# Optimization experiments

Measured on AMD Instinct MI355X. Metric: run time of the kernel, lower is better.

## Reference

```python
import jax, jax.numpy as jnp
import numpy as np

N = 20000   # nodes
E = 320000  # edges
F0 = 32     # num_features
H = 8       # GAT heads
G = 64      # graphs in batch


def setup_inputs() -> dict:
    key = jax.random.key(0)
    ks = jax.random.split(key, 16)
    def p(k, shape, s=0.05):
        return jax.random.normal(k, shape, jnp.float32) * s
    d = {}
    d['x'] = jax.random.normal(ks[0], (N, F0), jnp.float32)
    d['edge_index'] = jax.random.randint(ks[1], (2, E), 0, N, dtype=jnp.int32)
    d['edge_weights'] = jax.random.uniform(ks[2], (E,), jnp.float32)
    d['batch'] = jnp.sort(jax.random.randint(ks[3], (N,), 0, G, dtype=jnp.int32))
    # GATConv(32 -> 32, heads=8)
    d['W_gat'] = p(ks[4], (F0, H * F0)); d['att_src'] = p(ks[5], (H, F0))
    d['att_dst'] = p(ks[6], (H, F0));    d['b_gat'] = jnp.zeros((H * F0,), jnp.float32)
    # residual Linear(256 -> 1024) (widened so the residual add is shape-consistent)
    d['W_res'] = p(ks[7], (H * F0, 1024)); d['b_res'] = jnp.zeros((1024,), jnp.float32)
    # GCNConv(256 -> 512) + BN1
    d['W2'] = p(ks[8], (H * F0, 512)); d['b2'] = jnp.zeros((512,), jnp.float32)
    d['g1'] = jnp.ones((512,), jnp.float32); d['be1'] = jnp.zeros((512,), jnp.float32)
    d['m1'] = jnp.zeros((512,), jnp.float32); d['v1'] = jnp.ones((512,), jnp.float32)
    # GCNConv(512 -> 1024) + BN2
    d['W3'] = p(ks[9], (512, 1024)); d['b3'] = jnp.zeros((1024,), jnp.float32)
    d['g2'] = jnp.ones((1024,), jnp.float32); d['be2'] = jnp.zeros((1024,), jnp.float32)
    d['m2'] = jnp.zeros((1024,), jnp.float32); d['v2'] = jnp.ones((1024,), jnp.float32)
    # head
    d['Wf1'] = p(ks[10], (1024, 256)); d['bf1'] = jnp.zeros((256,), jnp.float32)
    d['Wf2'] = p(ks[11], (256, 2));    d['bf2'] = jnp.zeros((2,), jnp.float32)
    return d


def _add_self_loops(edge_index, edge_weight, n):
    loop = jnp.arange(n, dtype=edge_index.dtype)
    ei = jnp.concatenate([edge_index, jnp.stack([loop, loop])], axis=1)
    ew = jnp.concatenate([edge_weight, jnp.ones((n,), edge_weight.dtype)])
    return ei, ew


def _gat(x, edge_index, W, att_src, att_dst, b, n):
    # PyG GATConv, concat=True, eval (attention dropout off). Self-loops already added.
    src, dst = edge_index[0], edge_index[1]
    h = (x @ W).reshape(n, H, -1)                    # [N,H,C]
    a_s = jnp.einsum('nhc,hc->nh', h, att_src)        # [N,H]
    a_d = jnp.einsum('nhc,hc->nh', h, att_dst)
    e = jax.nn.leaky_relu(a_s[src] + a_d[dst], 0.2)   # [E,H]
    m = jax.ops.segment_max(e, dst, num_segments=n)   # softmax over incoming edges
    ex = jnp.exp(e - m[dst])
    s = jax.ops.segment_sum(ex, dst, num_segments=n)
    alpha = ex / s[dst]
    out = jax.ops.segment_sum(h[src] * alpha[:, :, None], dst, num_segments=n)
    return out.reshape(n, -1) + b                     # [N,H*C]


def _gcn(x, edge_index, w, W, b, n):
    # PyG GCNConv with symmetric normalization; self-loops (weight 1) already added.
    src, dst = edge_index[0], edge_index[1]
    deg = jax.ops.segment_sum(w, dst, num_segments=n)
    dinv = jnp.where(deg > 0, jax.lax.rsqrt(jnp.maximum(deg, 1e-12)), 0.0)
    norm = dinv[src] * w * dinv[dst]                  # [E]
    h = x @ W                                         # transform first (cheaper)
    return jax.ops.segment_sum(h[src] * norm[:, None], dst, num_segments=n) + b


def _bn(x, g, b, m, v):
    return g * (x - m) * jax.lax.rsqrt(v + 1e-5) + b


def reference(x, edge_index, edge_weights, batch, W_gat, att_src, att_dst, b_gat,
              W_res, b_res, W2, b2, g1, be1, m1, v1, W3, b3, g2, be2, m2, v2,
              Wf1, bf1, Wf2, bf2):
    n = x.shape[0]
    ei, ew = _add_self_loops(edge_index, edge_weights, n)
    h = jax.nn.relu(_gat(x, ei, W_gat, att_src, att_dst, b_gat, n))   # [N,256]
    res = h @ W_res + b_res                                           # [N,1024]
    h = _gcn(h, ei, ew, W2, b2, n)                                    # [N,512]
    h = jax.nn.relu(_bn(h, g1, be1, m1, v1))
    h = _gcn(h, ei, ew, W3, b3, n)                                    # [N,1024]
    h = jax.nn.relu(_bn(h, g2, be2, m2, v2))
    h = h + res
    pooled = jax.ops.segment_max(h, batch, num_segments=G)            # global max pool [G,1024]
    z = jax.nn.relu(pooled @ Wf1 + bf1)                               # dropout is eval no-op
    return z @ Wf2 + bf2                                              # [G,2]
```

## Files before the change

kernel.cpp:

```cpp
#include <hip/hip_runtime.h>
#include <hip/hip_bf16.h>

#define NN 20000
#define EE 320000
#define GG 64
#define EN (EE + NN)
#define MT 157

typedef float f32x4 __attribute__((ext_vector_type(4)));
typedef __bf16 bf16x4 __attribute__((ext_vector_type(4)));
typedef __bf16 bf16x8 __attribute__((ext_vector_type(8)));

__device__ __forceinline__ void gl_lds16(const void* g, void* l) {
    __builtin_amdgcn_global_load_lds((const __attribute__((address_space(1))) void*)g,
                                     (__attribute__((address_space(3))) void*)l, 16, 0, 0);
}

__global__ void sentinel_kernel(float* out, int n) {
    int i = blockIdx.x * 256 + threadIdx.x;
    if (i < n) out[i] = 12345.0f;
}

__global__ void init_kernel(int* deg_cnt, float* deg_w, int* fill, float* pooled) {
    int i = blockIdx.x * 256 + threadIdx.x;
    if (i < NN) { deg_cnt[i] = 1; deg_w[i] = 1.0f; fill[i] = 0; }
    if (i < GG * 1024) pooled[i] = -INFINITY;
}

__global__ __launch_bounds__(256) void convert_wt(const float* __restrict__ W, __bf16* __restrict__ Wt,
                                                  int K, int N) {
    __shared__ float tile[64][65];
    int kb = blockIdx.y * 64, nb = blockIdx.x * 64;
    int tx = threadIdx.x & 63, ty = threadIdx.x >> 6;
#pragma unroll
    for (int i = ty; i < 64; i += 4)
        tile[i][tx] = W[(size_t)(kb + i) * N + nb + tx];
    __syncthreads();
#pragma unroll
    for (int i = ty; i < 64; i += 4)
        Wt[(size_t)(nb + i) * K + kb + tx] = (__bf16)tile[tx][i];
}

__global__ __launch_bounds__(256) void gat_transform(
    const float* __restrict__ x, const float* __restrict__ W,
    const float* __restrict__ att_s, const float* __restrict__ att_d,
    __bf16* __restrict__ hlin, float* __restrict__ a_s, float* __restrict__ a_d)
{
    __shared__ float Ws[32 * 256];
    int tid = threadIdx.x;
#pragma unroll
    for (int k = 0; k < 32; k++) Ws[k * 256 + tid] = W[k * 256 + tid];
    float asc = att_s[tid], adc = att_d[tid];
    __syncthreads();
    for (int n = blockIdx.x; n < NN; n += gridDim.x) {
        const float* xp = x + (size_t)n * 32;
        float acc = 0.f;
#pragma unroll
        for (int k = 0; k < 32; k++) acc += xp[k] * Ws[k * 256 + tid];
        hlin[(size_t)n * 256 + tid] = (__bf16)acc;
        float s = acc * asc, d = acc * adc;
#pragma unroll
        for (int m = 1; m <= 16; m <<= 1) { s += __shfl_xor(s, m); d += __shfl_xor(d, m); }
        if ((tid & 31) == 0) { int h = tid >> 5; a_s[n * 8 + h] = s; a_d[n * 8 + h] = d; }
    }
}

__global__ void deg_kernel(const int* __restrict__ ei, const float* __restrict__ ew,
                           int* deg_cnt, float* deg_w) {
    int e = blockIdx.x * 256 + threadIdx.x;
    if (e >= EE) return;
    int dst = ei[EE + e];
    atomicAdd(&deg_cnt[dst], 1);
    atomicAdd(&deg_w[dst], ew[e]);
}

__global__ __launch_bounds__(256) void scan_kernel(const int* __restrict__ deg_cnt, int* __restrict__ rowptr) {
    __shared__ int partial[256];
    int tid = threadIdx.x;
    const int chunk = (NN + 255) / 256;
    int s0 = tid * chunk, s1 = min(s0 + chunk, NN);
    int sum = 0;
    for (int i = s0; i < s1; i++) sum += deg_cnt[i];
    partial[tid] = sum;
    __syncthreads();
    if (tid == 0) {
        int run = 0;
        for (int i = 0; i < 256; i++) { int t = partial[i]; partial[i] = run; run += t; }
        rowptr[NN] = run;
    }
    __syncthreads();
    int run = partial[tid];
    for (int i = s0; i < s1; i++) { rowptr[i] = run; run += deg_cnt[i]; }
}

__global__ void fill_kernel(const int* __restrict__ ei, const float* __restrict__ ew,
                            const float* __restrict__ deg_w, const int* __restrict__ rowptr,
                            int* fill, int* __restrict__ csr_src, float* __restrict__ csr_norm) {
    int e = blockIdx.x * 256 + threadIdx.x;
    if (e >= EN) return;
    int src, dst; float w;
    if (e < EE) { src = ei[e]; dst = ei[EE + e]; w = ew[e]; }
    else        { src = dst = e - EE; w = 1.0f; }
    int pos = atomicAdd(&fill[dst], 1);
    int slot = rowptr[dst] + pos;
    csr_src[slot] = src;
    csr_norm[slot] = rsqrtf(deg_w[src]) * w * rsqrtf(deg_w[dst]);
}

__global__ __launch_bounds__(256) void gat_agg(
    const int* __restrict__ rowptr, const int* __restrict__ csr_src,
    const float* __restrict__ a_s, const float* __restrict__ a_d,
    const __bf16* __restrict__ hlin, const float* __restrict__ b_gat,
    __bf16* __restrict__ h1)
{
    int widx = threadIdx.x >> 6, lane = threadIdx.x & 63;
    int node = blockIdx.x * 4 + widx;
    int base = rowptr[node], deg = rowptr[node + 1] - base;
    int hA = lane & 7;
    int eslot = lane >> 3;
    int hB = lane >> 3;
    float adA = a_d[node * 8 + hA];
    float acc0[4] = {0.f, 0.f, 0.f, 0.f};
    float acc1[4] = {0.f, 0.f, 0.f, 0.f};

    if (deg <= 64) {
        int sv = (lane < deg) ? csr_src[base + lane] : 0;
        float ev[8];
        float psum = 0.f;
#pragma unroll
        for (int j = 0; j < 8; j++) {
            int e = j * 8 + eslot;
            float v = 0.f;
            if (e < deg) {
                int src = __shfl(sv, e);
                float t = a_s[src * 8 + hA] + adA;
                t = (t > 0.f) ? t : 0.2f * t;
                v = __expf(t);
            }
            ev[j] = v;
            psum += v;
        }
#pragma unroll
        for (int m = 8; m <= 32; m <<= 1) psum += __shfl_xor(psum, m);
        float sinv = 1.f / __shfl(psum, hB);
#pragma unroll
        for (int j = 0; j < 8; j++) {
            if (j * 8 >= deg) break;
            int lim = min(8, deg - j * 8);
            int t = 0;
            for (; t + 1 < lim; t += 2) {
                int s0 = j * 8 + t, s1 = s0 + 1;
                int srcA = __shfl(sv, s0), srcB = __shfl(sv, s1);
                float aA = __shfl(ev[j], (t << 3) | hB) * sinv;
                float aB = __shfl(ev[j], ((t + 1) << 3) | hB) * sinv;
                bf16x4 fA = *(const bf16x4*)(hlin + (size_t)srcA * 256 + lane * 4);
                bf16x4 fB = *(const bf16x4*)(hlin + (size_t)srcB * 256 + lane * 4);
#pragma unroll
                for (int c = 0; c < 4; c++) { acc0[c] += aA * (float)fA[c]; acc1[c] += aB * (float)fB[c]; }
            }
            if (t < lim) {
                int s0 = j * 8 + t;
                int src = __shfl(sv, s0);
                float alpha = __shfl(ev[j], (t << 3) | hB) * sinv;
                bf16x4 f = *(const bf16x4*)(hlin + (size_t)src * 256 + lane * 4);
#pragma unroll
                for (int c = 0; c < 4; c++) acc0[c] += alpha * (float)f[c];
            }
        }
    } else {
        float sum = 0.f;
        for (int e = 0; e < deg; e++) {
            int src = csr_src[base + e];
            float t = a_s[src * 8 + hA] + adA;
            t = (t > 0.f) ? t : 0.2f * t;
            sum += __expf(t);
        }
        float sinv = 1.f / __shfl(sum, hB);
        float adB = a_d[node * 8 + hB];
        for (int e = 0; e < deg; e++) {
            int src = csr_src[base + e];
            float t = a_s[src * 8 + hB] + adB;
            t = (t > 0.f) ? t : 0.2f * t;
            float alpha = __expf(t) * sinv;
            bf16x4 f = *(const bf16x4*)(hlin + (size_t)src * 256 + lane * 4);
#pragma unroll
            for (int c = 0; c < 4; c++) acc0[c] += alpha * (float)f[c];
        }
    }
    float4 bg = *(const float4*)(b_gat + lane * 4);
    bf16x4 o;
    o[0] = (__bf16)fmaxf(acc0[0] + acc1[0] + bg.x, 0.f);
    o[1] = (__bf16)fmaxf(acc0[1] + acc1[1] + bg.y, 0.f);
    o[2] = (__bf16)fmaxf(acc0[2] + acc1[2] + bg.z, 0.f);
    o[3] = (__bf16)fmaxf(acc0[3] + acc1[3] + bg.w, 0.f);
    *(bf16x4*)(h1 + (size_t)node * 256 + lane * 4) = o;
}

template <int C, int SPLIT>
__global__ __launch_bounds__(256) void gcn_agg(
    const int* __restrict__ rowptr, const int* __restrict__ csr_src,
    const float* __restrict__ csr_norm, const __bf16* __restrict__ feat,
    __bf16* __restrict__ out)
{
    constexpr int V = C / (64 * SPLIT);
    int widx = threadIdx.x >> 6, lane = threadIdx.x & 63;
    int node = blockIdx.x * (4 / SPLIT) + widx / SPLIT;
    int half = widx % SPLIT;
    int coff = half * (C / SPLIT) + lane * V;
    int base = rowptr[node], deg = rowptr[node + 1] - base;
    float acc0[V], acc1[V], acc2[V], acc3[V];
#pragma unroll
    for (int j = 0; j < V; j++) { acc0[j] = 0.f; acc1[j] = 0.f; acc2[j] = 0.f; acc3[j] = 0.f; }
    const __bf16* fb = feat + coff;
    typedef __bf16 bf16v __attribute__((ext_vector_type(V)));
    for (int e0 = 0; e0 < deg; e0 += 64) {
        int cnt = min(64, deg - e0);
        int sv = 0; float wv = 0.f;
        if (lane < cnt) { sv = csr_src[base + e0 + lane]; wv = csr_norm[base + e0 + lane]; }
        int s = 0;
        for (; s + 3 < cnt; s += 4) {
            int sA = __shfl(sv, s),     sB = __shfl(sv, s + 1);
            int sC = __shfl(sv, s + 2), sD = __shfl(sv, s + 3);
            float wA = __shfl(wv, s),     wB = __shfl(wv, s + 1);
            float wC = __shfl(wv, s + 2), wD = __shfl(wv, s + 3);
            bf16v fA = *(const bf16v*)(fb + (size_t)sA * C);
            bf16v fB = *(const bf16v*)(fb + (size_t)sB * C);
            bf16v fC = *(const bf16v*)(fb + (size_t)sC * C);
            bf16v fD = *(const bf16v*)(fb + (size_t)sD * C);
#pragma unroll
            for (int j = 0; j < V; j++) {
                acc0[j] += wA * (float)fA[j]; acc1[j] += wB * (float)fB[j];
                acc2[j] += wC * (float)fC[j]; acc3[j] += wD * (float)fD[j];
            }
        }
        for (; s < cnt; s++) {
            int src = __shfl(sv, s);
            float w = __shfl(wv, s);
            bf16v f = *(const bf16v*)(fb + (size_t)src * C);
#pragma unroll
            for (int j = 0; j < V; j++) acc0[j] += w * (float)f[j];
        }
    }
    bf16v o;
#pragma unroll
    for (int j = 0; j < V; j++) o[j] = (__bf16)((acc0[j] + acc1[j]) + (acc2[j] + acc3[j]));
    *(bf16v*)(out + (size_t)node * C + coff) = o;
}


__device__ __forceinline__ void stage_async64(
    const __bf16* __restrict__ A, int K, const __bf16* __restrict__ Wt,
    int bm, int bn, int k0, int tid, __bf16* As, __bf16* Bs)
{
#pragma unroll
    for (int i = 0; i < 4; i++) {
        int j = i * 256 + tid;
        int r = j >> 3, c = j & 7;
        const __bf16* gp = A + (size_t)(bm + r) * K + k0 + ((c ^ (r & 7)) * 8);
        gl_lds16(gp, As + (size_t)(j & ~63) * 8);
    }
#pragma unroll
    for (int i = 0; i < 4; i++) {
        int j = i * 256 + tid;
        int r = j >> 3, c = j & 7;
        const __bf16* gp = Wt + (size_t)(bn + r) * K + k0 + ((c ^ (r & 7)) * 8);
        gl_lds16(gp, Bs + (size_t)(j & ~63) * 8);
    }
}

__device__ __forceinline__ void mfma_step64(
    const __bf16* As, const __bf16* Bs, int wr, int wc, int l16, int q, f32x4 (&acc)[4][4])
{
#pragma unroll
    for (int ks = 0; ks < 2; ks++) {
        bf16x8 af[4], bfv[4];
#pragma unroll
        for (int mt = 0; mt < 4; mt++) {
            int row = wr * 64 + mt * 16 + l16;
            af[mt] = *(const bf16x8*)(As + row * 64 + (((ks * 4 + q) ^ (row & 7)) * 8));
        }
#pragma unroll
        for (int nt = 0; nt < 4; nt++) {
            int row = wc * 64 + nt * 16 + l16;
            bfv[nt] = *(const bf16x8*)(Bs + row * 64 + (((ks * 4 + q) ^ (row & 7)) * 8));
        }
#pragma unroll
        for (int mt = 0; mt < 4; mt++)
#pragma unroll
            for (int nt = 0; nt < 4; nt++)
                acc[mt][nt] = __builtin_amdgcn_mfma_f32_16x16x32_bf16(af[mt], bfv[nt], acc[mt][nt], 0, 0, 0);
    }
}

__device__ __forceinline__ void gemm_loop(
    const __bf16* __restrict__ A, int K, const __bf16* __restrict__ Wt,
    int bm, int bn, int tid, int wr, int wc, int l16, int q,
    __bf16* As, __bf16* Bs, f32x4 (&acc)[4][4])
{
    for (int k0 = 0; k0 < K; k0 += 64) {
        stage_async64(A, K, Wt, bm, bn, k0, tid, As, Bs);
        __syncthreads();
        mfma_step64(As, Bs, wr, wc, l16, q, acc);
        __syncthreads();
    }
}

__global__ __launch_bounds__(256) void gemm_bn_relu(
    const __bf16* __restrict__ A, const __bf16* __restrict__ Wt,
    int M, int K, int Nc,
    const float* __restrict__ bias,
    const float* __restrict__ g, const float* __restrict__ be,
    const float* __restrict__ mu, const float* __restrict__ var,
    __bf16* __restrict__ C)
{
    __shared__ __bf16 As[128 * 64];
    __shared__ __bf16 Bs[128 * 64];
    int tid = threadIdx.x;
    int w = tid >> 6, wr = w >> 1, wc = w & 1;
    int l = tid & 63, q = l >> 4, l16 = l & 15;
    int i = blockIdx.x;
    int k = (i & 3) * MT + (i >> 2);
    int bm = (k >> 2) * 128, bn = (k & 3) * 128;
    f32x4 acc[4][4] = {};
    gemm_loop(A, K, Wt, bm, bn, tid, wr, wc, l16, q, As, Bs, acc);
#pragma unroll
    for (int nt = 0; nt < 4; nt++) {
        int gn = bn + wc * 64 + nt * 16 + l16;
        float s = g[gn] * rsqrtf(var[gn] + 1e-5f);
        float t = be[gn] - mu[gn] * s;
        float bv = bias[gn];
#pragma unroll
        for (int mt = 0; mt < 4; mt++)
#pragma unroll
            for (int r = 0; r < 4; r++) {
                int gm = bm + wr * 64 + mt * 16 + q * 4 + r;
                if (gm < M) C[(size_t)gm * Nc + gn] = (__bf16)fmaxf((acc[mt][nt][r] + bv) * s + t, 0.f);
            }
    }
}

__device__ __forceinline__ void atomicMaxFloat(float* addr, float value) {
    if (value >= 0.f) atomicMax((int*)addr, __float_as_int(value));
    else              atomicMin((unsigned int*)addr, __float_as_uint(value));
}

__global__ __launch_bounds__(256) void gemm_final(
    const __bf16* __restrict__ A1, const __bf16* __restrict__ W3t,
    const __bf16* __restrict__ A2, const __bf16* __restrict__ Wrt,
    const float* __restrict__ b3, const float* __restrict__ bres,
    const float* __restrict__ g, const float* __restrict__ be,
    const float* __restrict__ mu, const float* __restrict__ var,
    const int* __restrict__ batch, float* __restrict__ pooled)
{
    const int M = NN;
    __shared__ __bf16 As[128 * 64];
    __shared__ __bf16 Bs[128 * 64];
    __shared__ int bat[128];
    int tid = threadIdx.x;
    int w = tid >> 6, wr = w >> 1, wc = w & 1;
    int l = tid & 63, q = l >> 4, l16 = l & 15;
    int i = blockIdx.x;
    int k = (i & 7) * MT + (i >> 3);
    int bm = (k >> 3) * 128, bn = (k & 7) * 128;
    if (tid < 128) bat[tid] = (bm + tid < M) ? batch[bm + tid] : -1;
    f32x4 acc[4][4] = {};
    f32x4 accR[4][4] = {};
    gemm_loop(A1, 512, W3t, bm, bn, tid, wr, wc, l16, q, As, Bs, acc);
    gemm_loop(A2, 256, Wrt, bm, bn, tid, wr, wc, l16, q, As, Bs, accR);
#pragma unroll
    for (int nt = 0; nt < 4; nt++) {
        int gn = bn + wc * 64 + nt * 16 + l16;
        float s = g[gn] * rsqrtf(var[gn] + 1e-5f);
        float t = be[gn] - mu[gn] * s;
        float bv3 = b3[gn];
        float bvr = bres[gn];
        int cb = -1; float run = 0.f;
#pragma unroll
        for (int mt = 0; mt < 4; mt++)
#pragma unroll
            for (int r = 0; r < 4; r++) {
                int lr = wr * 64 + mt * 16 + q * 4 + r;
                int id = bat[lr];
                if (id < 0) continue;
                float v = fmaxf((acc[mt][nt][r] + bv3) * s + t, 0.f) + accR[mt][nt][r] + bvr;
                if (id == cb) run = fmaxf(run, v);
                else {
                    if (cb >= 0) atomicMaxFloat(&pooled[cb * 1024 + gn], run);
                    cb = id; run = v;
                }
            }
        if (cb >= 0) atomicMaxFloat(&pooled[cb * 1024 + gn], run);
    }
}

__global__ __launch_bounds__(256) void head_kernel(
    const float* __restrict__ pooled, const float* __restrict__ Wf1, const float* __restrict__ bf1,
    const float* __restrict__ Wf2, const float* __restrict__ bf2, float* __restrict__ out)
{
    int gph = blockIdx.x, tid = threadIdx.x;
    __shared__ float prow[1024];
    __shared__ float zred[256];
    for (int i = tid; i < 1024; i += 256) prow[i] = pooled[gph * 1024 + i];
    __syncthreads();
    float z = 0.f;
    for (int k = 0; k < 1024; k++) z += prow[k] * Wf1[k * 256 + tid];
    z = fmaxf(z + bf1[tid], 0.f);
    for (int c = 0; c < 2; c++) {
        zred[tid] = z * Wf2[tid * 2 + c];
        __syncthreads();
        for (int s = 128; s > 0; s >>= 1) { if (tid < s) zred[tid] += zred[tid + s]; __syncthreads(); }
        if (tid == 0) out[gph * 2 + c] = zred[0] + bf2[c];
        __syncthreads();
    }
}

extern "C" void kernel_launch(void* const* d_in, const int* in_sizes, int n_in,
                              void* d_out, int out_size, void* d_ws, size_t ws_size,
                              hipStream_t stream) {
    const float* x       = (const float*)d_in[0];
    const int*   ei      = (const int*)d_in[1];
    const float* ew      = (const float*)d_in[2];
    const int*   batch   = (const int*)d_in[3];
    const float* W_gat   = (const float*)d_in[4];
    const float* att_src = (const float*)d_in[5];
    const float* att_dst = (const float*)d_in[6];
    const float* b_gat   = (const float*)d_in[7];
    const float* W_res   = (const float*)d_in[8];
    const float* b_res   = (const float*)d_in[9];
    const float* W2      = (const float*)d_in[10];
    const float* b2v     = (const float*)d_in[11];
    const float* g1      = (const float*)d_in[12];
    const float* be1     = (const float*)d_in[13];
    const float* m1      = (const float*)d_in[14];
    const float* v1      = (const float*)d_in[15];
    const float* W3      = (const float*)d_in[16];
    const float* b3      = (const float*)d_in[17];
    const float* g2      = (const float*)d_in[18];
    const float* be2     = (const float*)d_in[19];
    const float* m2      = (const float*)d_in[20];
    const float* v2      = (const float*)d_in[21];
    const float* Wf1     = (const float*)d_in[22];
    const float* bf1     = (const float*)d_in[23];
    const float* Wf2     = (const float*)d_in[24];
    const float* bf2v    = (const float*)d_in[25];
    float* out           = (float*)d_out;

    char* ws = (char*)d_ws;
    size_t off = 0;
    auto alloc = [&](size_t bytes) { size_t o = off; off += (bytes + 255) & ~(size_t)255; return o; };
    size_t o_hlin   = alloc((size_t)NN * 256 * 2);
    size_t o_h1     = alloc((size_t)NN * 256 * 2);
    size_t o_h2     = alloc((size_t)NN * 512 * 2);
    size_t o_agg2   = alloc((size_t)NN * 512 * 2);
    size_t o_as     = alloc((size_t)NN * 8 * 4);
    size_t o_ad     = alloc((size_t)NN * 8 * 4);
    size_t o_degc   = alloc((size_t)NN * 4);
    size_t o_degw   = alloc((size_t)NN * 4);
    size_t o_rowptr = alloc((size_t)(NN + 1) * 4);
    size_t o_fill   = alloc((size_t)NN * 4);
    size_t o_csrs   = alloc((size_t)EN * 4);
    size_t o_csrn   = alloc((size_t)EN * 4);
    size_t o_pool   = alloc((size_t)GG * 1024 * 4);
    size_t o_w2t    = alloc((size_t)512 * 256 * 2);
    size_t o_w3t    = alloc((size_t)1024 * 512 * 2);
    size_t o_wrt    = alloc((size_t)1024 * 256 * 2);
    if (off > ws_size) {
        sentinel_kernel<<<(out_size + 255) / 256, 256, 0, stream>>>(out, out_size);
        return;
    }

    __bf16* hlin   = (__bf16*)(ws + o_hlin);
    __bf16* agg1   = hlin;
    __bf16* h1     = (__bf16*)(ws + o_h1);
    __bf16* h2     = (__bf16*)(ws + o_h2);
    __bf16* agg2   = (__bf16*)(ws + o_agg2);
    float*  a_s    = (float*)(ws + o_as);
    float*  a_d    = (float*)(ws + o_ad);
    int*    degc   = (int*)(ws + o_degc);
    float*  degw   = (float*)(ws + o_degw);
    int*    rowptr = (int*)(ws + o_rowptr);
    int*    fillb  = (int*)(ws + o_fill);
    int*    csrs   = (int*)(ws + o_csrs);
    float*  csrn   = (float*)(ws + o_csrn);
    float*  pooled = (float*)(ws + o_pool);
    __bf16* W2t    = (__bf16*)(ws + o_w2t);
    __bf16* W3t    = (__bf16*)(ws + o_w3t);
    __bf16* Wrt    = (__bf16*)(ws + o_wrt);

    init_kernel<<<256, 256, 0, stream>>>(degc, degw, fillb, pooled);
    convert_wt<<<dim3(512 / 64, 256 / 64), 256, 0, stream>>>(W2, W2t, 256, 512);
    convert_wt<<<dim3(1024 / 64, 512 / 64), 256, 0, stream>>>(W3, W3t, 512, 1024);
    convert_wt<<<dim3(1024 / 64, 256 / 64), 256, 0, stream>>>(W_res, Wrt, 256, 1024);

    gat_transform<<<512, 256, 0, stream>>>(x, W_gat, att_src, att_dst, hlin, a_s, a_d);
    deg_kernel<<<(EE + 255) / 256, 256, 0, stream>>>(ei, ew, degc, degw);
    scan_kernel<<<1, 256, 0, stream>>>(degc, rowptr);
    fill_kernel<<<(EN + 255) / 256, 256, 0, stream>>>(ei, ew, degw, rowptr, fillb, csrs, csrn);
    gat_agg<<<NN / 4, 256, 0, stream>>>(rowptr, csrs, a_s, a_d, hlin, b_gat, h1);

    gcn_agg<256, 1><<<NN / 4, 256, 0, stream>>>(rowptr, csrs, csrn, h1, agg1);
    gemm_bn_relu<<<4 * MT, 256, 0, stream>>>(agg1, W2t, NN, 256, 512, b2v,
        g1, be1, m1, v1, h2);
    gcn_agg<512, 2><<<NN / 2, 256, 0, stream>>>(rowptr, csrs, csrn, h2, agg2);
    gemm_final<<<8 * MT, 256, 0, stream>>>(agg2, W3t, h1, Wrt,
        b3, b_res, g2, be2, m2, v2, batch, pooled);

    head_kernel<<<GG, 256, 0, stream>>>(pooled, Wf1, bf1, Wf2, bf2v, out);
}
```

Before: 445.0 us.

## Fuse graph preprocessing into one cooperative kernel and merge weight conversions

Replaces the init, degree-count, scan and CSR-fill kernels with a single cooperative kernel that separates phases with grid-wide syncs, and parallelises the scan across 256 blocks instead of one. The three weight transpose/convert launches are merged into one launch that picks its matrix by block index. The aim is to cut kernel launch overhead and the serial single-block scan. In exchange it adds several grid barriers on a 256-block grid and limits the degree and fill loops to a fixed grid-stride launch.

Result: slower. 667.0 us (+49.9%).

```diff
diff --git a/kernel.cpp b/kernel.cpp
--- a/kernel.cpp
+++ b/kernel.cpp
@@ -1,11 +1,15 @@
 #include <hip/hip_runtime.h>
 #include <hip/hip_bf16.h>
+#include <hip/hip_cooperative_groups.h>
+
+namespace cg = cooperative_groups;
 
 #define NN 20000
 #define EE 320000
 #define GG 64
 #define EN (EE + NN)
 #define MT 157
+#define NPB 79
 
 typedef float f32x4 __attribute__((ext_vector_type(4)));
 typedef __bf16 bf16x4 __attribute__((ext_vector_type(4)));
@@ -21,16 +25,90 @@
     if (i < n) out[i] = 12345.0f;
 }
 
-__global__ void init_kernel(int* deg_cnt, float* deg_w, int* fill, float* pooled) {
-    int i = blockIdx.x * 256 + threadIdx.x;
-    if (i < NN) { deg_cnt[i] = 1; deg_w[i] = 1.0f; fill[i] = 0; }
-    if (i < GG * 1024) pooled[i] = -INFINITY;
-}
-
-__global__ __launch_bounds__(256) void convert_wt(const float* __restrict__ W, __bf16* __restrict__ Wt,
-                                                  int K, int N) {
+__global__ __launch_bounds__(256) void preproc_kernel(
+    int* __restrict__ deg_cnt, float* __restrict__ deg_w, int* __restrict__ fillc,
+    float* __restrict__ pooled,
+    const int* __restrict__ ei, const float* __restrict__ ew,
+    int* __restrict__ rowptr, int* __restrict__ bsum,
+    int* __restrict__ csr_src, float* __restrict__ csr_norm)
+{
+    cg::grid_group grid = cg::this_grid();
+    int tid = threadIdx.x, b = blockIdx.x;
+    int gtid = b * 256 + tid, gstride = 256 * 256;
+    __shared__ int red[256];
+    __shared__ int loc[NPB + 1];
+
+    for (int i = gtid; i < NN; i += gstride) { deg_cnt[i] = 1; deg_w[i] = 1.0f; fillc[i] = 0; }
+    for (int i = gtid; i < GG * 1024; i += gstride) pooled[i] = -INFINITY;
+    __threadfence();
+    grid.sync();
+
+    for (int e = gtid; e < EE; e += gstride) {
+        int dst = ei[EE + e];
+        atomicAdd(&deg_cnt[dst], 1);
+        atomicAdd(&deg_w[dst], ew[e]);
+    }
+    __threadfence();
+    grid.sync();
+
+    {
+        int s0 = b * NPB;
+        int v = 0;
+        if (tid < NPB && s0 + tid < NN) v = deg_cnt[s0 + tid];
+        red[tid] = v;
+        __syncthreads();
+        for (int s = 128; s > 0; s >>= 1) { if (tid < s) red[tid] += red[tid + s]; __syncthreads(); }
+        if (tid == 0) bsum[b] = red[0];
+    }
+    __threadfence();
+    grid.sync();
+
+    if (b == 0) {
+        if (tid == 0) {
+            int run = 0;
+            for (int i = 0; i < 256; i++) { int t = bsum[i]; bsum[i] = run; run += t; }
+            rowptr[NN] = run;
+        }
+    }
+    __threadfence();
+    grid.sync();
+
+    {
+        int s0 = b * NPB;
+        if (tid < NPB && s0 + tid < NN) loc[tid] = deg_cnt[s0 + tid];
+        __syncthreads();
+        if (tid == 0) {
+            int run = bsum[b];
+            for (int i = 0; i < NPB; i++) { int t = (s0 + i < NN) ? loc[i] : 0; loc[i] = run; run += t; }
+        }
+        __syncthreads();
+        if (tid < NPB && s0 + tid < NN) rowptr[s0 + tid] = loc[tid];
+    }
+    __threadfence();
+    grid.sync();
+
+    for (int e = gtid; e < EN; e += gstride) {
+        int src, dst; float w;
+        if (e < EE) { src = ei[e]; dst = ei[EE + e]; w = ew[e]; }
+        else        { src = dst = e - EE; w = 1.0f; }
+        int pos = atomicAdd(&fillc[dst], 1);
+        int slot = rowptr[dst] + pos;
+        csr_src[slot] = src;
+        csr_norm[slot] = rsqrtf(deg_w[src]) * w * rsqrtf(deg_w[dst]);
+    }
+}
+
+__global__ __launch_bounds__(256) void convert_all(
+    const float* __restrict__ W2, const float* __restrict__ W3, const float* __restrict__ Wres,
+    __bf16* __restrict__ W2t, __bf16* __restrict__ W3t, __bf16* __restrict__ Wrt)
+{
     __shared__ float tile[64][65];
-    int kb = blockIdx.y * 64, nb = blockIdx.x * 64;
+    int b = blockIdx.x;
+    const float* W; __bf16* Wt; int K, N, bx, by;
+    if (b < 32)       { W = W2;   Wt = W2t; K = 256; N = 512;  int bb = b;       bx = bb & 7;  by = bb >> 3; }
+    else if (b < 160) { W = W3;   Wt = W3t; K = 512; N = 1024; int bb = b - 32;  bx = bb & 15; by = bb >> 4; }
+    else              { W = Wres; Wt = Wrt; K = 256; N = 1024; int bb = b - 160; bx = bb & 15; by = bb >> 4; }
+    int kb = by * 64, nb = bx * 64;
     int tx = threadIdx.x & 63, ty = threadIdx.x >> 6;
 #pragma unroll
     for (int i = ty; i < 64; i += 4)
@@ -63,48 +141,6 @@
         for (int m = 1; m <= 16; m <<= 1) { s += __shfl_xor(s, m); d += __shfl_xor(d, m); }
         if ((tid & 31) == 0) { int h = tid >> 5; a_s[n * 8 + h] = s; a_d[n * 8 + h] = d; }
     }
-}
-
-__global__ void deg_kernel(const int* __restrict__ ei, const float* __restrict__ ew,
-                           int* deg_cnt, float* deg_w) {
-    int e = blockIdx.x * 256 + threadIdx.x;
-    if (e >= EE) return;
-    int dst = ei[EE + e];
-    atomicAdd(&deg_cnt[dst], 1);
-    atomicAdd(&deg_w[dst], ew[e]);
-}
-
-__global__ __launch_bounds__(256) void scan_kernel(const int* __restrict__ deg_cnt, int* __restrict__ rowptr) {
-    __shared__ int partial[256];
-    int tid = threadIdx.x;
-    const int chunk = (NN + 255) / 256;
-    int s0 = tid * chunk, s1 = min(s0 + chunk, NN);
-    int sum = 0;
-    for (int i = s0; i < s1; i++) sum += deg_cnt[i];
-    partial[tid] = sum;
-    __syncthreads();
-    if (tid == 0) {
-        int run = 0;
-        for (int i = 0; i < 256; i++) { int t = partial[i]; partial[i] = run; run += t; }
-        rowptr[NN] = run;
-    }
-    __syncthreads();
-    int run = partial[tid];
-    for (int i = s0; i < s1; i++) { rowptr[i] = run; run += deg_cnt[i]; }
-}
-
-__global__ void fill_kernel(const int* __restrict__ ei, const float* __restrict__ ew,
-                            const float* __restrict__ deg_w, const int* __restrict__ rowptr,
-                            int* fill, int* __restrict__ csr_src, float* __restrict__ csr_norm) {
-    int e = blockIdx.x * 256 + threadIdx.x;
-    if (e >= EN) return;
-    int src, dst; float w;
-    if (e < EE) { src = ei[e]; dst = ei[EE + e]; w = ew[e]; }
-    else        { src = dst = e - EE; w = 1.0f; }
-    int pos = atomicAdd(&fill[dst], 1);
-    int slot = rowptr[dst] + pos;
-    csr_src[slot] = src;
-    csr_norm[slot] = rsqrtf(deg_w[src]) * w * rsqrtf(deg_w[dst]);
 }
 
 __global__ __launch_bounds__(256) void gat_agg(
@@ -458,6 +494,7 @@
     size_t o_degw   = alloc((size_t)NN * 4);
     size_t o_rowptr = alloc((size_t)(NN + 1) * 4);
     size_t o_fill   = alloc((size_t)NN * 4);
+    size_t o_bsum   = alloc((size_t)256 * 4);
     size_t o_csrs   = alloc((size_t)EN * 4);
     size_t o_csrn   = alloc((size_t)EN * 4);
     size_t o_pool   = alloc((size_t)GG * 1024 * 4);
@@ -480,6 +517,7 @@
     float*  degw   = (float*)(ws + o_degw);
     int*    rowptr = (int*)(ws + o_rowptr);
     int*    fillb  = (int*)(ws + o_fill);
+    int*    bsum   = (int*)(ws + o_bsum);
     int*    csrs   = (int*)(ws + o_csrs);
     float*  csrn   = (float*)(ws + o_csrn);
     float*  pooled = (float*)(ws + o_pool);
@@ -487,15 +525,17 @@
     __bf16* W3t    = (__bf16*)(ws + o_w3t);
     __bf16* Wrt    = (__bf16*)(ws + o_wrt);
 
-    init_kernel<<<256, 256, 0, stream>>>(degc, degw, fillb, pooled);
-    convert_wt<<<dim3(512 / 64, 256 / 64), 256, 0, stream>>>(W2, W2t, 256, 512);
-    convert_wt<<<dim3(1024 / 64, 512 / 64), 256, 0, stream>>>(W3, W3t, 512, 1024);
-    convert_wt<<<dim3(1024 / 64, 256 / 64), 256, 0, stream>>>(W_res, Wrt, 256, 1024);
+    convert_all<<<224, 256, 0, stream>>>(W2, W3, W_res, W2t, W3t, Wrt);
 
     gat_transform<<<512, 256, 0, stream>>>(x, W_gat, att_src, att_dst, hlin, a_s, a_d);
-    deg_kernel<<<(EE + 255) / 256, 256, 0, stream>>>(ei, ew, degc, degw);
-    scan_kernel<<<1, 256, 0, stream>>>(degc, rowptr);
-    fill_kernel<<<(EN + 255) / 256, 256, 0, stream>>>(ei, ew, degw, rowptr, fillb, csrs, csrn);
+
+    {
+        void* args[] = { (void*)&degc, (void*)&degw, (void*)&fillb, (void*)&pooled,
+                         (void*)&ei, (void*)&ew, (void*)&rowptr, (void*)&bsum,
+                         (void*)&csrs, (void*)&csrn };
+        hipLaunchCooperativeKernel((void*)preproc_kernel, dim3(256), dim3(256), args, 0, stream);
+    }
+
     gat_agg<<<NN / 4, 256, 0, stream>>>(rowptr, csrs, a_s, a_d, hlin, b_gat, h1);
 
     gcn_agg<256, 1><<<NN / 4, 256, 0, stream>>>(rowptr, csrs, csrn, h1, agg1);
```

## Aggregate raw 32-dim inputs per head before GAT linear transform

Applied to the files above, without the earlier changes.

GAT attention scores are now computed by folding att_src/att_dst into W_gat (x·(W·att)), so the full 256-wide transformed features no longer need to be materialised before aggregation. The aggregation gathers the 32-float raw x rows per head instead of 256-wide bf16 hlin rows, and a new gat_post kernel applies the per-head W block, bias and ReLU afterwards. The three weight conversions are also merged into one launch. This cuts gather traffic per edge, at the cost of writing and reading an intermediate 256-wide per-node tensor plus an extra dense pass.

After: 439.3 us. No clear change (-1.3%).

```diff
diff --git a/kernel.cpp b/kernel.cpp
--- a/kernel.cpp
+++ b/kernel.cpp
@@ -25,44 +25,6 @@
     int i = blockIdx.x * 256 + threadIdx.x;
     if (i < NN) { deg_cnt[i] = 1; deg_w[i] = 1.0f; fill[i] = 0; }
     if (i < GG * 1024) pooled[i] = -INFINITY;
-}
-
-__global__ __launch_bounds__(256) void convert_wt(const float* __restrict__ W, __bf16* __restrict__ Wt,
-                                                  int K, int N) {
-    __shared__ float tile[64][65];
-    int kb = blockIdx.y * 64, nb = blockIdx.x * 64;
-    int tx = threadIdx.x & 63, ty = threadIdx.x >> 6;
-#pragma unroll
-    for (int i = ty; i < 64; i += 4)
-        tile[i][tx] = W[(size_t)(kb + i) * N + nb + tx];
-    __syncthreads();
-#pragma unroll
-    for (int i = ty; i < 64; i += 4)
-        Wt[(size_t)(nb + i) * K + kb + tx] = (__bf16)tile[tx][i];
-}
-
-__global__ __launch_bounds__(256) void gat_transform(
-    const float* __restrict__ x, const float* __restrict__ W,
-    const float* __restrict__ att_s, const float* __restrict__ att_d,
-    __bf16* __restrict__ hlin, float* __restrict__ a_s, float* __restrict__ a_d)
-{
-    __shared__ float Ws[32 * 256];
-    int tid = threadIdx.x;
-#pragma unroll
-    for (int k = 0; k < 32; k++) Ws[k * 256 + tid] = W[k * 256 + tid];
-    float asc = att_s[tid], adc = att_d[tid];
-    __syncthreads();
-    for (int n = blockIdx.x; n < NN; n += gridDim.x) {
-        const float* xp = x + (size_t)n * 32;
-        float acc = 0.f;
-#pragma unroll
-        for (int k = 0; k < 32; k++) acc += xp[k] * Ws[k * 256 + tid];
-        hlin[(size_t)n * 256 + tid] = (__bf16)acc;
-        float s = acc * asc, d = acc * adc;
-#pragma unroll
-        for (int m = 1; m <= 16; m <<= 1) { s += __shfl_xor(s, m); d += __shfl_xor(d, m); }
-        if ((tid & 31) == 0) { int h = tid >> 5; a_s[n * 8 + h] = s; a_d[n * 8 + h] = d; }
-    }
 }
 
 __global__ void deg_kernel(const int* __restrict__ ei, const float* __restrict__ ew,
@@ -107,21 +69,81 @@
     csr_norm[slot] = rsqrtf(deg_w[src]) * w * rsqrtf(deg_w[dst]);
 }
 
-__global__ __launch_bounds__(256) void gat_agg(
+__global__ __launch_bounds__(256) void convert_all(
+    const float* __restrict__ W2, const float* __restrict__ W3, const float* __restrict__ Wres,
+    __bf16* __restrict__ W2t, __bf16* __restrict__ W3t, __bf16* __restrict__ Wrt)
+{
+    __shared__ float tile[64][65];
+    int b = blockIdx.x;
+    const float* W; __bf16* Wt; int K, N, bx, by;
+    if (b < 32)       { W = W2;   Wt = W2t; K = 256; N = 512;  int bb = b;       bx = bb & 7;  by = bb >> 3; }
+    else if (b < 160) { W = W3;   Wt = W3t; K = 512; N = 1024; int bb = b - 32;  bx = bb & 15; by = bb >> 4; }
+    else              { W = Wres; Wt = Wrt; K = 256; N = 1024; int bb = b - 160; bx = bb & 15; by = bb >> 4; }
+    int kb = by * 64, nb = bx * 64;
+    int tx = threadIdx.x & 63, ty = threadIdx.x >> 6;
+#pragma unroll
+    for (int i = ty; i < 64; i += 4)
+        tile[i][tx] = W[(size_t)(kb + i) * N + nb + tx];
+    __syncthreads();
+#pragma unroll
+    for (int i = ty; i < 64; i += 4)
+        Wt[(size_t)(nb + i) * K + kb + tx] = (__bf16)tile[tx][i];
+}
+
+
+__global__ __launch_bounds__(256) void a_compute(
+    const float* __restrict__ x, const float* __restrict__ W,
+    const float* __restrict__ att_s, const float* __restrict__ att_d,
+    float* __restrict__ a_s, float* __restrict__ a_d)
+{
+    __shared__ float wss[8][32], wsd[8][32];
+    __shared__ float xs[32][33];
+    int tid = threadIdx.x;
+    {
+        int h = tid >> 5, k = tid & 31;
+        float s = 0.f, d = 0.f;
+#pragma unroll
+        for (int c = 0; c < 32; c++) {
+            float wv = W[k * 256 + h * 32 + c];
+            s += wv * att_s[h * 32 + c];
+            d += wv * att_d[h * 32 + c];
+        }
+        wss[h][k] = s; wsd[h][k] = d;
+    }
+    __syncthreads();
+    for (int n0 = blockIdx.x * 32; n0 < NN; n0 += gridDim.x * 32) {
+#pragma unroll
+        for (int i = 0; i < 4; i++) {
+            int idx = tid + i * 256;
+            xs[idx >> 5][idx & 31] = x[(size_t)n0 * 32 + idx];
+        }
+        __syncthreads();
+        int nl = tid >> 3, h = tid & 7;
+        float s = 0.f, d = 0.f;
+#pragma unroll
+        for (int k = 0; k < 32; k++) {
+            float xv = xs[nl][k];
+            s += xv * wss[h][k];
+            d += xv * wsd[h][k];
+        }
+        a_s[(n0 + nl) * 8 + h] = s;
+        a_d[(n0 + nl) * 8 + h] = d;
+        __syncthreads();
+    }
+}
+
+__global__ __launch_bounds__(256) void gat_agg_x(
     const int* __restrict__ rowptr, const int* __restrict__ csr_src,
     const float* __restrict__ a_s, const float* __restrict__ a_d,
-    const __bf16* __restrict__ hlin, const float* __restrict__ b_gat,
-    __bf16* __restrict__ h1)
+    const float* __restrict__ x, __bf16* __restrict__ xagg)
 {
     int widx = threadIdx.x >> 6, lane = threadIdx.x & 63;
     int node = blockIdx.x * 4 + widx;
     int base = rowptr[node], deg = rowptr[node + 1] - base;
-    int hA = lane & 7;
-    int eslot = lane >> 3;
-    int hB = lane >> 3;
+    int hA = lane & 7, eslot = lane >> 3;
+    int c = lane & 31, half = lane >> 5;
     float adA = a_d[node * 8 + hA];
-    float acc0[4] = {0.f, 0.f, 0.f, 0.f};
-    float acc1[4] = {0.f, 0.f, 0.f, 0.f};
+    float acc0[4] = {}, acc1[4] = {};
 
     if (deg <= 64) {
         int sv = (lane < deg) ? csr_src[base + lane] : 0;
@@ -142,29 +164,34 @@
         }
 #pragma unroll
         for (int m = 8; m <= 32; m <<= 1) psum += __shfl_xor(psum, m);
-        float sinv = 1.f / __shfl(psum, hB);
+        float sinv[4];
+#pragma unroll
+        for (int jj = 0; jj < 4; jj++) sinv[jj] = 1.f / __shfl(psum, half * 4 + jj);
 #pragma unroll
         for (int j = 0; j < 8; j++) {
             if (j * 8 >= deg) break;
             int lim = min(8, deg - j * 8);
             int t = 0;
             for (; t + 1 < lim; t += 2) {
-                int s0 = j * 8 + t, s1 = s0 + 1;
-                int srcA = __shfl(sv, s0), srcB = __shfl(sv, s1);
-                float aA = __shfl(ev[j], (t << 3) | hB) * sinv;
-                float aB = __shfl(ev[j], ((t + 1) << 3) | hB) * sinv;
-                bf16x4 fA = *(const bf16x4*)(hlin + (size_t)srcA * 256 + lane * 4);
-                bf16x4 fB = *(const bf16x4*)(hlin + (size_t)srcB * 256 + lane * 4);
-#pragma unroll
-                for (int c = 0; c < 4; c++) { acc0[c] += aA * (float)fA[c]; acc1[c] += aB * (float)fB[c]; }
+                int srcA = __shfl(sv, j * 8 + t), srcB = __shfl(sv, j * 8 + t + 1);
+                float xvA = x[(size_t)srcA * 32 + c];
+                float xvB = x[(size_t)srcB * 32 + c];
+#pragma unroll
+                for (int jj = 0; jj < 4; jj++) {
+                    float aA = __shfl(ev[j], (t << 3) | (half * 4 + jj)) * sinv[jj];
+                    float aB = __shfl(ev[j], ((t + 1) << 3) | (half * 4 + jj)) * sinv[jj];
+                    acc0[jj] += aA * xvA;
+                    acc1[jj] += aB * xvB;
+                }
             }
             if (t < lim) {
-                int s0 = j * 8 + t;
-                int src = __shfl(sv, s0);
-                float alpha = __shfl(ev[j], (t << 3) | hB) * sinv;
-                bf16x4 f = *(const bf16x4*)(hlin + (size_t)src * 256 + lane * 4);
-#pragma unroll
-                for (int c = 0; c < 4; c++) acc0[c] += alpha * (float)f[c];
+                int src = __shfl(sv, j * 8 + t);
+                float xv = x[(size_t)src * 32 + c];
+#pragma unroll
+                for (int jj = 0; jj < 4; jj++) {
+                    float a = __shfl(ev[j], (t << 3) | (half * 4 + jj)) * sinv[jj];
+                    acc0[jj] += a * xv;
+                }
             }
         }
     } else {
@@ -175,25 +202,49 @@
             t = (t > 0.f) ? t : 0.2f * t;
             sum += __expf(t);
         }
-        float sinv = 1.f / __shfl(sum, hB);
-        float adB = a_d[node * 8 + hB];
+        float sinv[4], ad4[4];
+#pragma unroll
+        for (int jj = 0; jj < 4; jj++) {
+            sinv[jj] = 1.f / __shfl(sum, half * 4 + jj);
+            ad4[jj] = a_d[node * 8 + half * 4 + jj];
+        }
         for (int e = 0; e < deg; e++) {
             int src = csr_src[base + e];
-            float t = a_s[src * 8 + hB] + adB;
-            t = (t > 0.f) ? t : 0.2f * t;
-            float alpha = __expf(t) * sinv;
-            bf16x4 f = *(const bf16x4*)(hlin + (size_t)src * 256 + lane * 4);
-#pragma unroll
-            for (int c = 0; c < 4; c++) acc0[c] += alpha * (float)f[c];
-        }
-    }
-    float4 bg = *(const float4*)(b_gat + lane * 4);
-    bf16x4 o;
-    o[0] = (__bf16)fmaxf(acc0[0] + acc1[0] + bg.x, 0.f);
-    o[1] = (__bf16)fmaxf(acc0[1] + acc1[1] + bg.y, 0.f);
-    o[2] = (__bf16)fmaxf(acc0[2] + acc1[2] + bg.z, 0.f);
-    o[3] = (__bf16)fmaxf(acc0[3] + acc1[3] + bg.w, 0.f);
-    *(bf16x4*)(h1 + (size_t)node * 256 + lane * 4) = o;
+            float xv = x[(size_t)src * 32 + c];
+#pragma unroll
+            for (int jj = 0; jj < 4; jj++) {
+                float t = a_s[src * 8 + half * 4 + jj] + ad4[jj];
+                t = (t > 0.f) ? t : 0.2f * t;
+                acc0[jj] += __expf(t) * sinv[jj] * xv;
+            }
+        }
+    }
+#pragma unroll
+    for (int jj = 0; jj < 4; jj++)
+        xagg[(size_t)node * 256 + (half * 4 + jj) * 32 + c] = (__bf16)(acc0[jj] + acc1[jj]);
+}
+
+__global__ __launch_bounds__(256) void gat_post(
+    const __bf16* __restrict__ xagg, const float* __restrict__ W,
+    const float* __restrict__ b_gat, __bf16* __restrict__ h1)
+{
+    __shared__ float Ws[32 * 256];
+    __shared__ float xr[256];
+    int tid = threadIdx.x;
+#pragma unroll
+    for (int k = 0; k < 32; k++) Ws[k * 256 + tid] = W[k * 256 + tid];
+    float bg = b_gat[tid];
+    int h = tid >> 5;
+    __syncthreads();
+    for (int n = blockIdx.x; n < NN; n += gridDim.x) {
+        xr[tid] = (float)xagg[(size_t)n * 256 + tid];
+        __syncthreads();
+        float acc = 0.f;
+#pragma unroll
+        for (int k = 0; k < 32; k++) acc += xr[h * 32 + k] * Ws[k * 256 + tid];
+        h1[(size_t)n * 256 + tid] = (__bf16)fmaxf(acc + bg, 0.f);
+        __syncthreads();
+    }
 }
 
 template <int C, int SPLIT>
@@ -469,8 +520,8 @@
         return;
     }
 
-    __bf16* hlin   = (__bf16*)(ws + o_hlin);
-    __bf16* agg1   = hlin;
+    __bf16* xagg   = (__bf16*)(ws + o_hlin);
+    __bf16* agg1   = xagg;
     __bf16* h1     = (__bf16*)(ws + o_h1);
     __bf16* h2     = (__bf16*)(ws + o_h2);
     __bf16* agg2   = (__bf16*)(ws + o_agg2);
@@ -487,16 +538,16 @@
     __bf16* W3t    = (__bf16*)(ws + o_w3t);
     __bf16* Wrt    = (__bf16*)(ws + o_wrt);
 
+    convert_all<<<224, 256, 0, stream>>>(W2, W3, W_res, W2t, W3t, Wrt);
+    a_compute<<<128, 256, 0, stream>>>(x, W_gat, att_src, att_dst, a_s, a_d);
+
     init_kernel<<<256, 256, 0, stream>>>(degc, degw, fillb, pooled);
-    convert_wt<<<dim3(512 / 64, 256 / 64), 256, 0, stream>>>(W2, W2t, 256, 512);
-    convert_wt<<<dim3(1024 / 64, 512 / 64), 256, 0, stream>>>(W3, W3t, 512, 1024);
-    convert_wt<<<dim3(1024 / 64, 256 / 64), 256, 0, stream>>>(W_res, Wrt, 256, 1024);
-
-    gat_transform<<<512, 256, 0, stream>>>(x, W_gat, att_src, att_dst, hlin, a_s, a_d);
     deg_kernel<<<(EE + 255) / 256, 256, 0, stream>>>(ei, ew, degc, degw);
     scan_kernel<<<1, 256, 0, stream>>>(degc, rowptr);
     fill_kernel<<<(EN + 255) / 256, 256, 0, stream>>>(ei, ew, degw, rowptr, fillb, csrs, csrn);
-    gat_agg<<<NN / 4, 256, 0, stream>>>(rowptr, csrs, a_s, a_d, hlin, b_gat, h1);
+
+    gat_agg_x<<<NN / 4, 256, 0, stream>>>(rowptr, csrs, a_s, a_d, x, xagg);
+    gat_post<<<512, 256, 0, stream>>>(xagg, W_gat, b_gat, h1);
 
     gcn_agg<256, 1><<<NN / 4, 256, 0, stream>>>(rowptr, csrs, csrn, h1, agg1);
     gemm_bn_relu<<<4 * MT, 256, 0, stream>>>(agg1, W2t, NN, 256, 512, b2v,
```
